# Performance work log

Hardware: AMD Instinct MI355X
Metric: run time of the kernel (lower is better)

The kernel has to match this reference:

```python
import jax, jax.numpy as jnp
import numpy as np

R0 = 5.0
LEAK = 0.1
N_NODES = 50000
N_EDGES = 1600000
DIM_A = 32
DIM_V = 32


def setup_inputs() -> dict:
    key = jax.random.key(0)
    ks = jax.random.split(key, 10)
    s = 1.0 / np.sqrt(DIM_A)
    return {
        "r_ij": jax.random.normal(ks[0], (N_EDGES, 3), dtype=jnp.float32) * 2.0,
        "res_emb": jax.random.normal(ks[1], (N_NODES, DIM_A), dtype=jnp.float32),
        "src": jax.random.randint(ks[2], (N_EDGES,), 0, N_NODES, dtype=jnp.int64),
        "dst": jax.random.randint(ks[3], (N_EDGES,), 0, N_NODES, dtype=jnp.int64),
        "W1": jax.random.normal(ks[4], (DIM_A, DIM_A), dtype=jnp.float32) * s,
        "b1": jnp.zeros((DIM_A,), dtype=jnp.float32),
        "W2": jax.random.normal(ks[5], (DIM_A, DIM_A), dtype=jnp.float32) * s,
        "b2": jnp.zeros((DIM_A,), dtype=jnp.float32),
        "W3": jax.random.normal(ks[6], (DIM_A, DIM_A), dtype=jnp.float32) * s,
        "Wv": jax.random.normal(ks[7], (DIM_V, DIM_A), dtype=jnp.float32) * s,
    }


def _radial_encode(r, n, rmax):
    # r: [E, 3] -> [E, n]
    hn = (n + 1) // 2
    coeffs = (jnp.pi / rmax) * (1 + jnp.arange(hn) // 2).astype(r.dtype)
    dist = jnp.linalg.norm(r, axis=-1)[..., None]  # [E, 1]
    phase = coeffs * dist                           # [E, hn]
    return jnp.concatenate([jnp.cos(phase), jnp.sin(phase[..., : n - hn])], axis=-1)


def _leaky(x):
    return jnp.where(x >= 0, x, LEAK * x)


def _tens_sigmoid_vec(x):
    # Equivariant saturating nonlinearity on vectors: scale by tanh(|x|)/|x|.
    nrm = jnp.linalg.norm(x, axis=-1, keepdims=True)
    safe = jnp.where(nrm > 0, nrm, 1.0)
    return x * (jnp.tanh(nrm) / safe)


def reference(r_ij, res_emb, src, dst, W1, b1, W2, b2, W3, Wv):
    n_nodes = res_emb.shape[0]
    dim_a = W1.shape[1]
    # gather dst node features onto edges
    res_emb_j = res_emb[dst]                              # [E, dim_a]
    x = _radial_encode(r_ij, dim_a, R0) + res_emb_j       # [E, dim_a]
    h = _leaky(x @ W1.T + b1)
    h = _leaky(h @ W2.T + b2)
    rad_enc_ij = h @ W3.T                                 # [E, dim_a]
    rv = _tens_sigmoid_vec(r_ij * (7.0 / R0))             # [E, 3]
    phi_v = rad_enc_ij[..., None] * rv[:, None, :]        # [E, dim_a, 3]
    A_a = jax.ops.segment_sum(rad_enc_ij, src, num_segments=n_nodes)  # [N, dim_a]
    A_v = jax.ops.segment_sum(phi_v, src, num_segments=n_nodes)       # [N, dim_a, 3]
    out_v = jnp.einsum("nad,va->nvd", A_v, Wv)            # [N, dim_v, 3]
    return A_a, out_v
```

## Files before the change

### kernel.cpp

```cpp
#include <hip/hip_runtime.h>
#include <math.h>


#define NN 50000
#define NE 1600000
#define DA 32
#define PI_R0 0.62831853071795864769f
#define SCAN_BLOCKS 196

typedef float v2f __attribute__((ext_vector_type(2)));
typedef short bf16x8 __attribute__((ext_vector_type(8)));
typedef float f32x16 __attribute__((ext_vector_type(16)));

union frag_u { unsigned u[4]; bf16x8 v; };

__device__ __forceinline__ void wsync() {
    asm volatile("s_waitcnt lgkmcnt(0)" ::: "memory");
}

__device__ __forceinline__ unsigned cvt_pk(float lo, float hi) {
    unsigned r;
    asm("v_cvt_pk_bf16_f32 %0, %1, %2" : "=v"(r) : "v"(lo), "v"(hi));
    return r;
}

__device__ __forceinline__ float leaky(float x) {
    return fmaxf(x, 0.0f) + 0.1f * fminf(x, 0.0f);
}

__device__ __forceinline__ unsigned bf_hi(float x) {
    return (__float_as_uint(x) + 0x8000u) >> 16;
}
__device__ __forceinline__ unsigned bf_pack2(float lo, float hi) {
    return bf_hi(lo) | ((__float_as_uint(hi) + 0x8000u) & 0xffff0000u);
}


__global__ __launch_bounds__(256) void k_hist(const int* __restrict__ src,
                                              int* __restrict__ counts,
                                              int* __restrict__ rank) {
    const int e = blockIdx.x * 256 + threadIdx.x;
    rank[e] = atomicAdd(&counts[src[e]], 1);
}

__global__ __launch_bounds__(256) void k_scanA(const int* __restrict__ counts,
                                               int* __restrict__ bsum) {
    __shared__ int red[256];
    const int t = threadIdx.x;
    const int idx = blockIdx.x * 256 + t;
    red[t] = (idx < NN) ? counts[idx] : 0;
    __syncthreads();
    #pragma unroll
    for (int off = 128; off > 0; off >>= 1) {
        if (t < off) red[t] += red[t + off];
        __syncthreads();
    }
    if (t == 0) bsum[blockIdx.x] = red[0];
}

__global__ __launch_bounds__(256) void k_scanB(const int* __restrict__ bsum,
                                               int* __restrict__ bbase) {
    __shared__ int s[256];
    const int t = threadIdx.x;
    const int v = (t < SCAN_BLOCKS) ? bsum[t] : 0;
    s[t] = v;
    __syncthreads();
    #pragma unroll
    for (int off = 1; off < 256; off <<= 1) {
        const int x = s[t] + ((t >= off) ? s[t - off] : 0);
        __syncthreads();
        s[t] = x;
        __syncthreads();
    }
    if (t < SCAN_BLOCKS) bbase[t] = s[t] - v;
}

__global__ __launch_bounds__(256) void k_scanC(const int* __restrict__ counts,
                                               const int* __restrict__ bbase,
                                               int* __restrict__ offsets) {
    __shared__ int s[256];
    const int t = threadIdx.x;
    const int idx = blockIdx.x * 256 + t;
    const int v = (idx < NN) ? counts[idx] : 0;
    s[t] = v;
    __syncthreads();
    #pragma unroll
    for (int off = 1; off < 256; off <<= 1) {
        const int x = s[t] + ((t >= off) ? s[t - off] : 0);
        __syncthreads();
        s[t] = x;
        __syncthreads();
    }
    const int excl = s[t] - v + bbase[blockIdx.x];
    if (idx < NN) offsets[idx] = excl;
    if (idx == NN - 1) offsets[NN] = excl + v;
}

__global__ __launch_bounds__(256) void k_prep(
    const float* __restrict__ r_ij,
    const int*   __restrict__ src,
    const int*   __restrict__ dst,
    const int*   __restrict__ offsets,
    const int*   __restrict__ rank,
    uint4* __restrict__ rec)
{
    const int e = blockIdx.x * 256 + threadIdx.x;
    const int s = src[e];
    const int slot = offsets[s] + rank[e];

    const float rx = r_ij[(size_t)e*3 + 0];
    const float ry = r_ij[(size_t)e*3 + 1];
    const float rz = r_ij[(size_t)e*3 + 2];
    const float dist = sqrtf(rx*rx + ry*ry + rz*rz);

    const float nq = 1.4f * dist;
    const float e2 = __expf(2.0f * nq);
    const float sc14 = (nq > 0.0f)
        ? 1.4f * (e2 - 1.0f) * __builtin_amdgcn_rcpf((e2 + 1.0f) * nq)
        : 0.0f;

    uint4 r;
    r.x = __float_as_uint(dist);
    r.y = bf_pack2(rx * sc14, ry * sc14);
    r.z = bf_hi(rz * sc14);
    r.w = (unsigned)s | ((unsigned)dst[e] << 16);
    rec[slot] = r;
}

__global__ __launch_bounds__(256) void k_embcvt(const float* __restrict__ emb,
                                                unsigned* __restrict__ emb16) {
    const int t = blockIdx.x * 256 + threadIdx.x;
    emb16[t] = bf_pack2(emb[2*t], emb[2*t + 1]);
}


__global__ __launch_bounds__(256, 2) void dt_window(
    const uint4*    __restrict__ rec,
    const unsigned* __restrict__ emb16,
    const float* __restrict__ W1, const float* __restrict__ b1,
    const float* __restrict__ W2, const float* __restrict__ b2,
    const float* __restrict__ W3,
    float* __restrict__ A_a,
    float* __restrict__ out_v)
{
    __shared__ float  xrad[4][64][36];
    __shared__ float4 rvn_lds[4][64];

    const int tid  = threadIdx.x;
    const int wv   = tid >> 6;
    const int lane = tid & 63;
    const int g    = lane >> 5;
    const int m    = lane & 31;
    const int slot = blockIdx.x * 256 + tid;

    frag_u wf1[2], wf2[2], wf3[2];
    #pragma unroll
    for (int kt = 0; kt < 2; ++kt) {
        const float4 a1 = *(const float4*)&W1[m*DA + 16*kt + 4*g];
        const float4 c1 = *(const float4*)&W1[m*DA + 16*kt + 8 + 4*g];
        wf1[kt].u[0] = cvt_pk(a1.x, a1.y); wf1[kt].u[1] = cvt_pk(a1.z, a1.w);
        wf1[kt].u[2] = cvt_pk(c1.x, c1.y); wf1[kt].u[3] = cvt_pk(c1.z, c1.w);
        const float4 a2 = *(const float4*)&W2[m*DA + 16*kt + 4*g];
        const float4 c2 = *(const float4*)&W2[m*DA + 16*kt + 8 + 4*g];
        wf2[kt].u[0] = cvt_pk(a2.x, a2.y); wf2[kt].u[1] = cvt_pk(a2.z, a2.w);
        wf2[kt].u[2] = cvt_pk(c2.x, c2.y); wf2[kt].u[3] = cvt_pk(c2.z, c2.w);
        const float4 a3 = *(const float4*)&W3[m*DA + 16*kt + 4*g];
        const float4 c3 = *(const float4*)&W3[m*DA + 16*kt + 8 + 4*g];
        wf3[kt].u[0] = cvt_pk(a3.x, a3.y); wf3[kt].u[1] = cvt_pk(a3.z, a3.w);
        wf3[kt].u[2] = cvt_pk(c3.x, c3.y); wf3[kt].u[3] = cvt_pk(c3.z, c3.w);
    }

    const float4 b1q0 = *(const float4*)&b1[4*g];
    const float4 b1q1 = *(const float4*)&b1[8 + 4*g];
    const float4 b1q2 = *(const float4*)&b1[16 + 4*g];
    const float4 b1q3 = *(const float4*)&b1[24 + 4*g];
    const float4 b2q0 = *(const float4*)&b2[4*g];
    const float4 b2q1 = *(const float4*)&b2[8 + 4*g];
    const float4 b2q2 = *(const float4*)&b2[16 + 4*g];
    const float4 b2q3 = *(const float4*)&b2[24 + 4*g];

    const uint4 rc = rec[slot];
    const float dist = __uint_as_float(rc.x);
    const float vx = __uint_as_float(rc.y << 16);
    const float vy = __uint_as_float(rc.y & 0xffff0000u);
    const float vz = __uint_as_float(rc.z << 16);
    const int  node = (int)(rc.w & 0xffffu);
    const int  dn   = (int)(rc.w >> 16);

    v2f xa[16];
    #pragma unroll
    for (int mm = 0; mm < 8; ++mm) {
        float sph, cph;
        __sincosf(PI_R0 * (float)(mm + 1) * dist, &sph, &cph);
        xa[mm]     = (v2f){cph, cph};
        xa[8 + mm] = (v2f){sph, sph};
    }
    const uint4* ep = (const uint4*)(emb16 + (size_t)dn * 16);
    #pragma unroll
    for (int q = 0; q < 4; ++q) {
        const uint4 u = ep[q];
        xa[q*4 + 0] += (v2f){__uint_as_float(u.x << 16), __uint_as_float(u.x & 0xffff0000u)};
        xa[q*4 + 1] += (v2f){__uint_as_float(u.y << 16), __uint_as_float(u.y & 0xffff0000u)};
        xa[q*4 + 2] += (v2f){__uint_as_float(u.z << 16), __uint_as_float(u.z & 0xffff0000u)};
        xa[q*4 + 3] += (v2f){__uint_as_float(u.w << 16), __uint_as_float(u.w & 0xffff0000u)};
    }

    rvn_lds[wv][lane] = make_float4(vx, vy, vz, __int_as_float(node));

    {
        unsigned* xr = (unsigned*)&xrad[wv][lane][0];
        uint4 w0, w1_, w2_, w3_;
        w0.x  = cvt_pk(xa[0].x,  xa[0].y);  w0.y  = cvt_pk(xa[1].x,  xa[1].y);
        w0.z  = cvt_pk(xa[2].x,  xa[2].y);  w0.w  = cvt_pk(xa[3].x,  xa[3].y);
        w1_.x = cvt_pk(xa[4].x,  xa[4].y);  w1_.y = cvt_pk(xa[5].x,  xa[5].y);
        w1_.z = cvt_pk(xa[6].x,  xa[6].y);  w1_.w = cvt_pk(xa[7].x,  xa[7].y);
        w2_.x = cvt_pk(xa[8].x,  xa[8].y);  w2_.y = cvt_pk(xa[9].x,  xa[9].y);
        w2_.z = cvt_pk(xa[10].x, xa[10].y); w2_.w = cvt_pk(xa[11].x, xa[11].y);
        w3_.x = cvt_pk(xa[12].x, xa[12].y); w3_.y = cvt_pk(xa[13].x, xa[13].y);
        w3_.z = cvt_pk(xa[14].x, xa[14].y); w3_.w = cvt_pk(xa[15].x, xa[15].y);
        ((uint4*)xr)[0] = w0; ((uint4*)xr)[1] = w1_;
        ((uint4*)xr)[2] = w2_; ((uint4*)xr)[3] = w3_;
    }
    wsync();

    frag_u xf[2][2];
    #pragma unroll
    for (int t = 0; t < 2; ++t) {
        const unsigned* er = (const unsigned*)&xrad[wv][32*t + m][0];
        #pragma unroll
        for (int kt = 0; kt < 2; ++kt) {
            const uint2 qa = *(const uint2*)&er[8*kt + 2*g];
            const uint2 qb = *(const uint2*)&er[8*kt + 4 + 2*g];
            xf[t][kt].u[0] = qa.x; xf[t][kt].u[1] = qa.y;
            xf[t][kt].u[2] = qb.x; xf[t][kt].u[3] = qb.y;
        }
    }

    f32x16 acc0, acc1;
    acc0[0]=b1q0.x; acc0[1]=b1q0.y; acc0[2]=b1q0.z; acc0[3]=b1q0.w;
    acc0[4]=b1q1.x; acc0[5]=b1q1.y; acc0[6]=b1q1.z; acc0[7]=b1q1.w;
    acc0[8]=b1q2.x; acc0[9]=b1q2.y; acc0[10]=b1q2.z; acc0[11]=b1q2.w;
    acc0[12]=b1q3.x; acc0[13]=b1q3.y; acc0[14]=b1q3.z; acc0[15]=b1q3.w;
    acc1 = acc0;
    acc0 = __builtin_amdgcn_mfma_f32_32x32x16_bf16(wf1[0].v, xf[0][0].v, acc0, 0, 0, 0);
    acc0 = __builtin_amdgcn_mfma_f32_32x32x16_bf16(wf1[1].v, xf[0][1].v, acc0, 0, 0, 0);
    acc1 = __builtin_amdgcn_mfma_f32_32x32x16_bf16(wf1[0].v, xf[1][0].v, acc1, 0, 0, 0);
    acc1 = __builtin_amdgcn_mfma_f32_32x32x16_bf16(wf1[1].v, xf[1][1].v, acc1, 0, 0, 0);

    frag_u hf[2][2];
    #pragma unroll
    for (int t = 0; t < 2; ++t) {
        const f32x16 a = t ? acc1 : acc0;
        float h[16];
        #pragma unroll
        for (int r = 0; r < 16; ++r) h[r] = leaky(a[r]);
        hf[t][0].u[0] = cvt_pk(h[0], h[1]);   hf[t][0].u[1] = cvt_pk(h[2], h[3]);
        hf[t][0].u[2] = cvt_pk(h[4], h[5]);   hf[t][0].u[3] = cvt_pk(h[6], h[7]);
        hf[t][1].u[0] = cvt_pk(h[8], h[9]);   hf[t][1].u[1] = cvt_pk(h[10], h[11]);
        hf[t][1].u[2] = cvt_pk(h[12], h[13]); hf[t][1].u[3] = cvt_pk(h[14], h[15]);
    }

    f32x16 c0, c1;
    c0[0]=b2q0.x; c0[1]=b2q0.y; c0[2]=b2q0.z; c0[3]=b2q0.w;
    c0[4]=b2q1.x; c0[5]=b2q1.y; c0[6]=b2q1.z; c0[7]=b2q1.w;
    c0[8]=b2q2.x; c0[9]=b2q2.y; c0[10]=b2q2.z; c0[11]=b2q2.w;
    c0[12]=b2q3.x; c0[13]=b2q3.y; c0[14]=b2q3.z; c0[15]=b2q3.w;
    c1 = c0;
    c0 = __builtin_amdgcn_mfma_f32_32x32x16_bf16(wf2[0].v, hf[0][0].v, c0, 0, 0, 0);
    c0 = __builtin_amdgcn_mfma_f32_32x32x16_bf16(wf2[1].v, hf[0][1].v, c0, 0, 0, 0);
    c1 = __builtin_amdgcn_mfma_f32_32x32x16_bf16(wf2[0].v, hf[1][0].v, c1, 0, 0, 0);
    c1 = __builtin_amdgcn_mfma_f32_32x32x16_bf16(wf2[1].v, hf[1][1].v, c1, 0, 0, 0);

    frag_u gf[2][2];
    #pragma unroll
    for (int t = 0; t < 2; ++t) {
        const f32x16 a = t ? c1 : c0;
        float h[16];
        #pragma unroll
        for (int r = 0; r < 16; ++r) h[r] = leaky(a[r]);
        gf[t][0].u[0] = cvt_pk(h[0], h[1]);   gf[t][0].u[1] = cvt_pk(h[2], h[3]);
        gf[t][0].u[2] = cvt_pk(h[4], h[5]);   gf[t][0].u[3] = cvt_pk(h[6], h[7]);
        gf[t][1].u[0] = cvt_pk(h[8], h[9]);   gf[t][1].u[1] = cvt_pk(h[10], h[11]);
        gf[t][1].u[2] = cvt_pk(h[12], h[13]); gf[t][1].u[3] = cvt_pk(h[14], h[15]);
    }

    f32x16 r0 = {}, r1 = {};
    r0 = __builtin_amdgcn_mfma_f32_32x32x16_bf16(wf3[0].v, gf[0][0].v, r0, 0, 0, 0);
    r0 = __builtin_amdgcn_mfma_f32_32x32x16_bf16(wf3[1].v, gf[0][1].v, r0, 0, 0, 0);
    r1 = __builtin_amdgcn_mfma_f32_32x32x16_bf16(wf3[0].v, gf[1][0].v, r1, 0, 0, 0);
    r1 = __builtin_amdgcn_mfma_f32_32x32x16_bf16(wf3[1].v, gf[1][1].v, r1, 0, 0, 0);

    #pragma unroll
    for (int t = 0; t < 2; ++t) {
        const f32x16 a = t ? r1 : r0;
        float* rr = &xrad[wv][32*t + m][0];
        *(float4*)&rr[4*g]      = make_float4(a[0],  a[1],  a[2],  a[3]);
        *(float4*)&rr[8 + 4*g]  = make_float4(a[4],  a[5],  a[6],  a[7]);
        *(float4*)&rr[16 + 4*g] = make_float4(a[8],  a[9],  a[10], a[11]);
        *(float4*)&rr[24 + 4*g] = make_float4(a[12], a[13], a[14], a[15]);
    }
    wsync();

    const int p = lane >> 5;
    const int i = lane & 31;

    float accA = 0.0f, a0 = 0.0f, a1 = 0.0f, a2 = 0.0f;
    int cur = __float_as_int(rvn_lds[wv][0].w);

    #pragma unroll 4
    for (int l = 0; l < 64; ++l) {
        const float4 rvn = rvn_lds[wv][l];
        const int nd = __float_as_int(rvn.w);
        const float rd = xrad[wv][l][i];
        if (nd != cur) {
            if (p == 0) {
                atomicAdd(&A_a[cur*DA + i], accA);
                atomicAdd(&out_v[(cur*DA + i)*3 + 0], a0);
            } else {
                atomicAdd(&out_v[(cur*DA + i)*3 + 1], a1);
                atomicAdd(&out_v[(cur*DA + i)*3 + 2], a2);
            }
            accA = a0 = a1 = a2 = 0.0f;
            cur = nd;
        }
        accA += rd;
        a0 += rd * rvn.x;
        a1 += rd * rvn.y;
        a2 += rd * rvn.z;
    }
    if (p == 0) {
        atomicAdd(&A_a[cur*DA + i], accA);
        atomicAdd(&out_v[(cur*DA + i)*3 + 0], a0);
    } else {
        atomicAdd(&out_v[(cur*DA + i)*3 + 1], a1);
        atomicAdd(&out_v[(cur*DA + i)*3 + 2], a2);
    }
}


__global__ __launch_bounds__(256) void dt_node(
    const float* __restrict__ Wv,
    float* Av_out)
{
    __shared__ float sWv[DA*DA];
    for (int i = threadIdx.x; i < DA*DA; i += 256) sWv[i] = Wv[i];
    __syncthreads();

    const int t = blockIdx.x * 256 + threadIdx.x;
    const int n = t >> 5;
    const int v = t & 31;

    const float* av = Av_out + (size_t)n * (DA*3);
    float o0 = 0.0f, o1 = 0.0f, o2 = 0.0f;
    #pragma unroll
    for (int a = 0; a < DA; ++a) {
        const float w = sWv[v*DA + a];
        o0 += w * av[a*3 + 0];
        o1 += w * av[a*3 + 1];
        o2 += w * av[a*3 + 2];
    }
    __syncthreads();
    float* o = Av_out + (size_t)n * (DA*3) + v*3;
    o[0] = o0; o[1] = o1; o[2] = o2;
}


__global__ __launch_bounds__(256) void k_scan_legacy(const int* __restrict__ counts,
                                                     int* __restrict__ offsets) {
    __shared__ int part[256];
    const int CH = (NN + 255) / 256;
    const int t = threadIdx.x;
    const int base = t * CH;
    int s = 0;
    for (int k = 0; k < CH; ++k) { const int idx = base + k; if (idx < NN) s += counts[idx]; }
    part[t] = s;
    __syncthreads();
    if (t == 0) {
        int run = 0;
        for (int k = 0; k < 256; ++k) { const int v = part[k]; part[k] = run; run += v; }
    }
    __syncthreads();
    int run = part[t];
    for (int k = 0; k < CH; ++k) {
        const int idx = base + k;
        if (idx < NN) { offsets[idx] = run; run += counts[idx]; }
    }
    if (t == 255) offsets[NN] = run;
}

__global__ __launch_bounds__(256) void k_scatter_legacy(const int* __restrict__ src,
                                                        const int* __restrict__ offsets,
                                                        const int* __restrict__ rank,
                                                        int* __restrict__ edge_ids) {
    const int e = blockIdx.x * 256 + threadIdx.x;
    edge_ids[offsets[src[e]] + rank[e]] = e;
}

__global__ __launch_bounds__(256, 2) void dt_window_legacy(
    const float* __restrict__ r_ij,
    const float* __restrict__ res_emb,
    const int*   __restrict__ src,
    const int*   __restrict__ dst,
    const int*   __restrict__ edge_ids,
    const float* __restrict__ W1, const float* __restrict__ b1,
    const float* __restrict__ W2, const float* __restrict__ b2,
    const float* __restrict__ W3,
    float* __restrict__ A_a,
    float* __restrict__ out_v)
{
    __shared__ float  rad_lds[4][32][36];
    __shared__ float4 rvn_lds[4][64];

    const int tid  = threadIdx.x;
    const int wv   = tid >> 6;
    const int lane = tid & 63;
    const int slot = blockIdx.x * 256 + tid;

    const int eid  = edge_ids[slot];
    const int node = src[eid];

    const float rx = r_ij[(size_t)eid*3 + 0];
    const float ry = r_ij[(size_t)eid*3 + 1];
    const float rz = r_ij[(size_t)eid*3 + 2];
    const float dist = sqrtf(rx*rx + ry*ry + rz*rz);

    float xa[DA], xb[DA];
    #pragma unroll
    for (int mm = 0; mm < 8; ++mm) {
        float sph, cph;
        __sincosf(PI_R0 * (float)(mm + 1) * dist, &sph, &cph);
        xa[2*mm] = cph; xa[2*mm+1] = cph;
        xa[16+2*mm] = sph; xa[16+2*mm+1] = sph;
    }
    const float4* er = (const float4*)(res_emb + (size_t)dst[eid] * DA);
    #pragma unroll
    for (int q = 0; q < 8; ++q) {
        const float4 v = er[q];
        xa[q*4+0] += v.x; xa[q*4+1] += v.y; xa[q*4+2] += v.z; xa[q*4+3] += v.w;
    }
    #pragma unroll
    for (int i = 0; i < DA; ++i) {
        float acc = b1[i];
        #pragma unroll
        for (int j = 0; j < DA; ++j) acc += W1[i*DA + j] * xa[j];
        xb[i] = (acc >= 0.0f) ? acc : 0.1f * acc;
    }
    #pragma unroll
    for (int i = 0; i < DA; ++i) {
        float acc = b2[i];
        #pragma unroll
        for (int j = 0; j < DA; ++j) acc += W2[i*DA + j] * xb[j];
        xa[i] = (acc >= 0.0f) ? acc : 0.1f * acc;
    }
    #pragma unroll
    for (int i = 0; i < DA; ++i) {
        float acc = 0.0f;
        #pragma unroll
        for (int j = 0; j < DA; ++j) acc += W3[i*DA + j] * xa[j];
        xb[i] = acc;
    }

    const float qx = rx*1.4f, qy = ry*1.4f, qz = rz*1.4f;
    const float nq = sqrtf(qx*qx + qy*qy + qz*qz);
    const float e2 = __expf(2.0f * nq);
    const float sc = (nq > 0.0f)
        ? (e2 - 1.0f) * __builtin_amdgcn_rcpf((e2 + 1.0f) * nq)
        : 0.0f;

    rvn_lds[wv][lane] = make_float4(qx*sc, qy*sc, qz*sc, __int_as_float(node));

    const int p = lane >> 5;
    const int i = lane & 31;

    if (lane < 32) {
        float* rrow = rad_lds[wv][lane];
        #pragma unroll
        for (int q = 0; q < 8; ++q)
            *(float4*)&rrow[q*4] = make_float4(xb[q*4+0], xb[q*4+1], xb[q*4+2], xb[q*4+3]);
    }
    wsync();

    float accA = 0.0f, a0 = 0.0f, a1 = 0.0f, a2 = 0.0f;
    int cur = __float_as_int(rvn_lds[wv][0].w);

    #pragma unroll 4
    for (int l = 0; l < 32; ++l) {
        const float4 rvn = rvn_lds[wv][l];
        const int nd = __float_as_int(rvn.w);
        const float rd = rad_lds[wv][l][i];
        if (nd != cur) {
            if (p == 0) {
                atomicAdd(&A_a[cur*DA + i], accA);
                atomicAdd(&out_v[(cur*DA + i)*3 + 0], a0);
            } else {
                atomicAdd(&out_v[(cur*DA + i)*3 + 1], a1);
                atomicAdd(&out_v[(cur*DA + i)*3 + 2], a2);
            }
            accA = a0 = a1 = a2 = 0.0f;
            cur = nd;
        }
        accA += rd; a0 += rd*rvn.x; a1 += rd*rvn.y; a2 += rd*rvn.z;
    }
    wsync();
    if (lane >= 32) {
        float* rrow = rad_lds[wv][lane - 32];
        #pragma unroll
        for (int q = 0; q < 8; ++q)
            *(float4*)&rrow[q*4] = make_float4(xb[q*4+0], xb[q*4+1], xb[q*4+2], xb[q*4+3]);
    }
    wsync();
    #pragma unroll 4
    for (int l = 32; l < 64; ++l) {
        const float4 rvn = rvn_lds[wv][l];
        const int nd = __float_as_int(rvn.w);
        const float rd = rad_lds[wv][l - 32][i];
        if (nd != cur) {
            if (p == 0) {
                atomicAdd(&A_a[cur*DA + i], accA);
                atomicAdd(&out_v[(cur*DA + i)*3 + 0], a0);
            } else {
                atomicAdd(&out_v[(cur*DA + i)*3 + 1], a1);
                atomicAdd(&out_v[(cur*DA + i)*3 + 2], a2);
            }
            accA = a0 = a1 = a2 = 0.0f;
            cur = nd;
        }
        accA += rd; a0 += rd*rvn.x; a1 += rd*rvn.y; a2 += rd*rvn.z;
    }
    if (p == 0) {
        atomicAdd(&A_a[cur*DA + i], accA);
        atomicAdd(&out_v[(cur*DA + i)*3 + 0], a0);
    } else {
        atomicAdd(&out_v[(cur*DA + i)*3 + 1], a1);
        atomicAdd(&out_v[(cur*DA + i)*3 + 2], a2);
    }
}


extern "C" void kernel_launch(void* const* d_in, const int* in_sizes, int n_in,
                              void* d_out, int out_size, void* d_ws, size_t ws_size,
                              hipStream_t stream) {
    const float* r_ij    = (const float*)d_in[0];
    const float* res_emb = (const float*)d_in[1];
    const int*   src     = (const int*)d_in[2];
    const int*   dst     = (const int*)d_in[3];
    const float* W1      = (const float*)d_in[4];
    const float* b1      = (const float*)d_in[5];
    const float* W2      = (const float*)d_in[6];
    const float* b2      = (const float*)d_in[7];
    const float* W3      = (const float*)d_in[8];
    const float* Wv      = (const float*)d_in[9];

    float* A_a   = (float*)d_out;
    float* out_v = (float*)d_out + (size_t)NN * DA;

    const size_t need_new = ((size_t)NE*4 + (size_t)NN*16 + NN + NN + 1 + NE + 256 + 256) * sizeof(int);
    const size_t need_leg = ((size_t)NN + NN + 1 + NE + NE) * sizeof(int);

    hipMemsetAsync(d_out, 0, (size_t)out_size * sizeof(float), stream);

    if (ws_size >= need_new) {
        uint4*    rec     = (uint4*)d_ws;
        unsigned* emb16   = (unsigned*)(rec + NE);
        int*      counts  = (int*)(emb16 + (size_t)NN*16);
        int*      offsets = counts + NN;
        int*      rank    = offsets + NN + 1;
        int*      bsum    = rank + NE;
        int*      bbase   = bsum + 256;

        hipMemsetAsync(counts, 0, (size_t)NN * sizeof(int), stream);
        k_hist  <<<NE / 256, 256, 0, stream>>>(src, counts, rank);
        k_scanA <<<SCAN_BLOCKS, 256, 0, stream>>>(counts, bsum);
        k_scanB <<<1, 256, 0, stream>>>(bsum, bbase);
        k_scanC <<<SCAN_BLOCKS, 256, 0, stream>>>(counts, bbase, offsets);
        k_embcvt<<<(NN*16) / 256, 256, 0, stream>>>(res_emb, emb16);
        k_prep  <<<NE / 256, 256, 0, stream>>>(r_ij, src, dst, offsets, rank, rec);
        dt_window<<<NE / 256, 256, 0, stream>>>(rec, emb16,
                                                W1, b1, W2, b2, W3, A_a, out_v);
        dt_node <<<(NN * DA) / 256, 256, 0, stream>>>(Wv, out_v);
    } else if (ws_size >= need_leg) {
        int* counts   = (int*)d_ws;
        int* offsets  = counts + NN;
        int* rank     = offsets + NN + 1;
        int* edge_ids = rank + NE;

        hipMemsetAsync(counts, 0, (size_t)NN * sizeof(int), stream);
        k_hist          <<<NE / 256, 256, 0, stream>>>(src, counts, rank);
        k_scan_legacy   <<<1, 256, 0, stream>>>(counts, offsets);
        k_scatter_legacy<<<NE / 256, 256, 0, stream>>>(src, offsets, rank, edge_ids);
        dt_window_legacy<<<NE / 256, 256, 0, stream>>>(r_ij, res_emb, src, dst, edge_ids,
                                                       W1, b1, W2, b2, W3, A_a, out_v);
        dt_node         <<<(NN * DA) / 256, 256, 0, stream>>>(Wv, out_v);
    }
}
```

Before: 248.7 us.

## Pad LDS row stride to 34 and split segment scan across half-waves

```diff
diff --git a/kernel.cpp b/kernel.cpp
--- a/kernel.cpp
+++ b/kernel.cpp
@@ -7,6 +7,7 @@
 #define DA 32
 #define PI_R0 0.62831853071795864769f
 #define SCAN_BLOCKS 196
+#define RSTRIDE 34
 
 typedef float v2f __attribute__((ext_vector_type(2)));
 typedef short bf16x8 __attribute__((ext_vector_type(8)));
@@ -143,7 +144,7 @@
     float* __restrict__ A_a,
     float* __restrict__ out_v)
 {
-    __shared__ float  xrad[4][64][36];
+    __shared__ float  xrad[4][64][RSTRIDE];
     __shared__ float4 rvn_lds[4][64];
 
     const int tid  = threadIdx.x;
@@ -208,18 +209,15 @@
     rvn_lds[wv][lane] = make_float4(vx, vy, vz, __int_as_float(node));
 
     {
-        unsigned* xr = (unsigned*)&xrad[wv][lane][0];
-        uint4 w0, w1_, w2_, w3_;
-        w0.x  = cvt_pk(xa[0].x,  xa[0].y);  w0.y  = cvt_pk(xa[1].x,  xa[1].y);
-        w0.z  = cvt_pk(xa[2].x,  xa[2].y);  w0.w  = cvt_pk(xa[3].x,  xa[3].y);
-        w1_.x = cvt_pk(xa[4].x,  xa[4].y);  w1_.y = cvt_pk(xa[5].x,  xa[5].y);
-        w1_.z = cvt_pk(xa[6].x,  xa[6].y);  w1_.w = cvt_pk(xa[7].x,  xa[7].y);
-        w2_.x = cvt_pk(xa[8].x,  xa[8].y);  w2_.y = cvt_pk(xa[9].x,  xa[9].y);
-        w2_.z = cvt_pk(xa[10].x, xa[10].y); w2_.w = cvt_pk(xa[11].x, xa[11].y);
-        w3_.x = cvt_pk(xa[12].x, xa[12].y); w3_.y = cvt_pk(xa[13].x, xa[13].y);
-        w3_.z = cvt_pk(xa[14].x, xa[14].y); w3_.w = cvt_pk(xa[15].x, xa[15].y);
-        ((uint4*)xr)[0] = w0; ((uint4*)xr)[1] = w1_;
-        ((uint4*)xr)[2] = w2_; ((uint4*)xr)[3] = w3_;
+        uint2* xr = (uint2*)&xrad[wv][lane][0];
+        xr[0] = make_uint2(cvt_pk(xa[0].x,  xa[0].y),  cvt_pk(xa[1].x,  xa[1].y));
+        xr[1] = make_uint2(cvt_pk(xa[2].x,  xa[2].y),  cvt_pk(xa[3].x,  xa[3].y));
+        xr[2] = make_uint2(cvt_pk(xa[4].x,  xa[4].y),  cvt_pk(xa[5].x,  xa[5].y));
+        xr[3] = make_uint2(cvt_pk(xa[6].x,  xa[6].y),  cvt_pk(xa[7].x,  xa[7].y));
+        xr[4] = make_uint2(cvt_pk(xa[8].x,  xa[8].y),  cvt_pk(xa[9].x,  xa[9].y));
+        xr[5] = make_uint2(cvt_pk(xa[10].x, xa[10].y), cvt_pk(xa[11].x, xa[11].y));
+        xr[6] = make_uint2(cvt_pk(xa[12].x, xa[12].y), cvt_pk(xa[13].x, xa[13].y));
+        xr[7] = make_uint2(cvt_pk(xa[14].x, xa[14].y), cvt_pk(xa[15].x, xa[15].y));
     }
     wsync();
 
@@ -294,32 +292,34 @@
     for (int t = 0; t < 2; ++t) {
         const f32x16 a = t ? r1 : r0;
         float* rr = &xrad[wv][32*t + m][0];
-        *(float4*)&rr[4*g]      = make_float4(a[0],  a[1],  a[2],  a[3]);
-        *(float4*)&rr[8 + 4*g]  = make_float4(a[4],  a[5],  a[6],  a[7]);
-        *(float4*)&rr[16 + 4*g] = make_float4(a[8],  a[9],  a[10], a[11]);
-        *(float4*)&rr[24 + 4*g] = make_float4(a[12], a[13], a[14], a[15]);
+        *(float2*)&rr[4*g]          = make_float2(a[0],  a[1]);
+        *(float2*)&rr[4*g + 2]      = make_float2(a[2],  a[3]);
+        *(float2*)&rr[8 + 4*g]      = make_float2(a[4],  a[5]);
+        *(float2*)&rr[8 + 4*g + 2]  = make_float2(a[6],  a[7]);
+        *(float2*)&rr[16 + 4*g]     = make_float2(a[8],  a[9]);
+        *(float2*)&rr[16 + 4*g + 2] = make_float2(a[10], a[11]);
+        *(float2*)&rr[24 + 4*g]     = make_float2(a[12], a[13]);
+        *(float2*)&rr[24 + 4*g + 2] = make_float2(a[14], a[15]);
     }
     wsync();
 
     const int p = lane >> 5;
     const int i = lane & 31;
+    const int base = p << 5;
 
     float accA = 0.0f, a0 = 0.0f, a1 = 0.0f, a2 = 0.0f;
-    int cur = __float_as_int(rvn_lds[wv][0].w);
+    int cur = __float_as_int(rvn_lds[wv][base].w);
 
     #pragma unroll 4
-    for (int l = 0; l < 64; ++l) {
-        const float4 rvn = rvn_lds[wv][l];
+    for (int l = 0; l < 32; ++l) {
+        const float4 rvn = rvn_lds[wv][base + l];
         const int nd = __float_as_int(rvn.w);
-        const float rd = xrad[wv][l][i];
+        const float rd = xrad[wv][base + l][i];
         if (nd != cur) {
-            if (p == 0) {
-                atomicAdd(&A_a[cur*DA + i], accA);
-                atomicAdd(&out_v[(cur*DA + i)*3 + 0], a0);
-            } else {
-                atomicAdd(&out_v[(cur*DA + i)*3 + 1], a1);
-                atomicAdd(&out_v[(cur*DA + i)*3 + 2], a2);
-            }
+            atomicAdd(&A_a[cur*DA + i], accA);
+            atomicAdd(&out_v[(cur*DA + i)*3 + 0], a0);
+            atomicAdd(&out_v[(cur*DA + i)*3 + 1], a1);
+            atomicAdd(&out_v[(cur*DA + i)*3 + 2], a2);
             accA = a0 = a1 = a2 = 0.0f;
             cur = nd;
         }
@@ -328,13 +328,10 @@
         a1 += rd * rvn.y;
         a2 += rd * rvn.z;
     }
-    if (p == 0) {
-        atomicAdd(&A_a[cur*DA + i], accA);
-        atomicAdd(&out_v[(cur*DA + i)*3 + 0], a0);
-    } else {
-        atomicAdd(&out_v[(cur*DA + i)*3 + 1], a1);
-        atomicAdd(&out_v[(cur*DA + i)*3 + 2], a2);
-    }
+    atomicAdd(&A_a[cur*DA + i], accA);
+    atomicAdd(&out_v[(cur*DA + i)*3 + 0], a0);
+    atomicAdd(&out_v[(cur*DA + i)*3 + 1], a1);
+    atomicAdd(&out_v[(cur*DA + i)*3 + 2], a2);
 }
 
 
```

Measured after the change: 260.1 us. 4.6% more time.
